# Kernel optimization log

Measured on AMD Instinct MI355X. Metric: run time of the kernel, lower is better.

The kernel has to match this reference:

```python
import jax, jax.numpy as jnp
import numpy as np

NEG_INF = -1e30


def _rotate_half(t):
    d = t.shape[-1] // 2
    t1, t2 = t[..., :d], t[..., d:]
    return jnp.concatenate([-t2, t1], axis=-1)


def _apply_rope(t, cos, sin):
    # t: [B, H, T, D]; cos/sin: [T, D] broadcast over B, H
    return t * cos[None, None, :, :] + _rotate_half(t) * sin[None, None, :, :]


def setup_inputs() -> dict:
    key = jax.random.key(0)
    ks = jax.random.split(key, 5)
    B, T, C, H = 2, 2048, 2048, 16
    D = C // H
    x = jax.random.normal(ks[0], (B, T, C), dtype=jnp.float32)
    # RoPE tables (realistic: derived from inv freqs)
    inv_freq = 1.0 / (10000.0 ** (jnp.arange(0, D, 2, dtype=jnp.float32) / D))
    freqs = jnp.arange(T, dtype=jnp.float32)[:, None] * inv_freq[None, :]
    emb = jnp.concatenate([freqs, freqs], axis=-1)  # [T, D]
    cos, sin = jnp.cos(emb), jnp.sin(emb)
    W_attn = jax.random.normal(ks[1], (C, 3 * C), dtype=jnp.float32) * (1.0 / np.sqrt(C))
    W_proj = jax.random.normal(ks[2], (C, C), dtype=jnp.float32) * (1.0 / np.sqrt(C))
    return {"x": x, "cos": cos, "sin": sin, "W_attn": W_attn, "W_proj": W_proj}


def reference(x, cos, sin, W_attn, W_proj):
    B, T, C = x.shape
    H = 16
    D = C // H
    qkv = x @ W_attn  # [B, T, 3C]
    q, k, v = jnp.split(qkv, 3, axis=-1)
    # [B, T, C] -> [B, H, T, D]
    to_heads = lambda t: t.reshape(B, T, H, D).transpose(0, 2, 1, 3)
    q, k, v = to_heads(q), to_heads(k), to_heads(v)
    q = _apply_rope(q, cos, sin)
    k = _apply_rope(k, cos, sin)
    scale = 1.0 / np.sqrt(D).astype(np.float32)
    scores = jnp.einsum("bhqd,bhkd->bhqk", q, k) * scale
    causal = jnp.tril(jnp.ones((T, T), dtype=bool))
    scores = jnp.where(causal[None, None, :, :], scores, NEG_INF)
    attn = jax.nn.softmax(scores, axis=-1)
    out = jnp.einsum("bhqk,bhkd->bhqd", attn, v)  # [B, H, T, D]
    out = out.transpose(0, 2, 1, 3).reshape(B, T, C)
    return out @ W_proj
```

## Files before the change

### kernel.cpp

```cpp
#include <hip/hip_runtime.h>
#include <stdint.h>

#define Bc   2
#define Tc   2048
#define Cc   2048
#define Hc   16
#define Dc   128
#define BT   4096
#define N3   6144
#define QSCALE 0.08838834764831845f

typedef _Float16 f16x8 __attribute__((ext_vector_type(8)));
typedef _Float16 f16x4 __attribute__((ext_vector_type(4)));
typedef float    f32x4 __attribute__((ext_vector_type(4)));

__device__ __forceinline__ void gload_lds16(const void* g, void* l) {
  __builtin_amdgcn_global_load_lds(
      (__attribute__((address_space(1))) void*)(uintptr_t)g,
      (__attribute__((address_space(3))) void*)(unsigned int)(uintptr_t)l,
      16, 0, 0);
}

__global__ __launch_bounds__(256) void cvt_f16_kernel(const float* __restrict__ in,
                                                      _Float16* __restrict__ out, int n4) {
  int i = blockIdx.x * 256 + threadIdx.x;
  if (i < n4) {
    float4 v = ((const float4*)in)[i];
    f16x4 o; o[0]=(_Float16)v.x; o[1]=(_Float16)v.y; o[2]=(_Float16)v.z; o[3]=(_Float16)v.w;
    ((f16x4*)out)[i] = o;
  }
}

__global__ __launch_bounds__(256) void transpose_cvt_kernel(const float* __restrict__ W,
                                                            _Float16* __restrict__ Wt,
                                                            int K, int N) {
  const int n0 = blockIdx.x * 64, k0 = blockIdx.y * 64;
  __shared__ float tile[64][65];
  const int tid = threadIdx.x;
  #pragma unroll
  for (int i = 0; i < 4; ++i) {
    int u = i * 256 + tid, r = u >> 4, s = u & 15;
    float4 v = *(const float4*)&W[(size_t)(k0 + r) * N + n0 + s * 4];
    tile[r][s*4+0] = v.x; tile[r][s*4+1] = v.y; tile[r][s*4+2] = v.z; tile[r][s*4+3] = v.w;
  }
  __syncthreads();
  #pragma unroll
  for (int i = 0; i < 2; ++i) {
    int u = i * 256 + tid, c = u >> 3, rg = u & 7;
    f16x8 o;
    #pragma unroll
    for (int j = 0; j < 8; ++j) o[j] = (_Float16)tile[rg * 8 + j][c];
    *(f16x8*)&Wt[(size_t)(n0 + c) * K + k0 + rg * 8] = o;
  }
}

#define GLDS_BUF 49152

template<bool OUT16>
__global__ __launch_bounds__(512, 1) void gemm256_kernel(const _Float16* __restrict__ A,
                                                         const _Float16* __restrict__ Bt,
                                                         void* __restrict__ C,
                                                         int M, int N, int K) {
  __shared__ __align__(16) char glds[3 * GLDS_BUF];
  const int tid = threadIdx.x;
  const int wid = tid >> 6, lane = tid & 63, g = lane >> 4, c16 = lane & 15;
  const int wr = wid >> 1, wc = wid & 1;

  const int nblocks = gridDim.x, chunk = nblocks >> 3;
  const int bid = blockIdx.x;
  const int sw = (bid & 7) * chunk + (bid >> 3);
  const int ntm = M >> 8;
  const int m0 = (sw % ntm) * 256, n0 = (sw / ntm) * 128;

  const int ntk = K >> 6;
  const int row8 = tid >> 3, s8 = tid & 7;
  const int scol = (s8 ^ (row8 & 7)) * 8;
  const int swz = (c16 & 7) << 4;

  auto stage_tile = [&](char* bb, int kt) {
    #pragma unroll
    for (int c = 0; c < 4; ++c)
      gload_lds16(A + (size_t)(m0 + c * 64 + row8) * K + kt * 64 + scol,
                  bb + c * 8192 + tid * 16);
    #pragma unroll
    for (int c = 0; c < 2; ++c)
      gload_lds16(Bt + (size_t)(n0 + c * 64 + row8) * K + kt * 64 + scol,
                  bb + 32768 + c * 8192 + tid * 16);
  };

  f32x4 acc[4][4] = {};

  char* p0 = glds;
  char* p1 = glds + GLDS_BUF;
  char* p2 = glds + 2 * GLDS_BUF;
  stage_tile(p0, 0);
  stage_tile(p1, 1);

  for (int t = 0; t < ntk; ++t) {
    if (t < ntk - 1) asm volatile("s_waitcnt vmcnt(6)" ::: "memory");
    else             asm volatile("s_waitcnt vmcnt(0)" ::: "memory");
    __builtin_amdgcn_s_barrier();

    f16x8 a0[4], b0[4];
    #pragma unroll
    for (int mi = 0; mi < 4; ++mi)
      a0[mi] = *(const f16x8*)(p0 + (wr * 64 + mi * 16 + c16) * 128 + ((g * 16) ^ swz));
    #pragma unroll
    for (int ni = 0; ni < 4; ++ni)
      b0[ni] = *(const f16x8*)(p0 + 32768 + (wc * 64 + ni * 16 + c16) * 128 + ((g * 16) ^ swz));
    __builtin_amdgcn_s_setprio(1);
    #pragma unroll
    for (int mi = 0; mi < 4; ++mi)
      #pragma unroll
      for (int ni = 0; ni < 4; ++ni)
        acc[mi][ni] = __builtin_amdgcn_mfma_f32_16x16x32_f16(a0[mi], b0[ni], acc[mi][ni], 0, 0, 0);
    __builtin_amdgcn_s_setprio(0);
    asm volatile("s_waitcnt lgkmcnt(0)" ::: "memory");
    __builtin_amdgcn_sched_barrier(0);
    __builtin_amdgcn_s_barrier();

    if (t + 2 < ntk) stage_tile(p2, t + 2);

    f16x8 a1[4], b1[4];
    #pragma unroll
    for (int mi = 0; mi < 4; ++mi)
      a1[mi] = *(const f16x8*)(p0 + (wr * 64 + mi * 16 + c16) * 128 + ((64 + g * 16) ^ swz));
    #pragma unroll
    for (int ni = 0; ni < 4; ++ni)
      b1[ni] = *(const f16x8*)(p0 + 32768 + (wc * 64 + ni * 16 + c16) * 128 + ((64 + g * 16) ^ swz));
    __builtin_amdgcn_s_setprio(1);
    #pragma unroll
    for (int mi = 0; mi < 4; ++mi)
      #pragma unroll
      for (int ni = 0; ni < 4; ++ni)
        acc[mi][ni] = __builtin_amdgcn_mfma_f32_16x16x32_f16(a1[mi], b1[ni], acc[mi][ni], 0, 0, 0);
    __builtin_amdgcn_s_setprio(0);
    asm volatile("s_waitcnt lgkmcnt(0)" ::: "memory");
    __builtin_amdgcn_sched_barrier(0);

    char* tp = p0; p0 = p1; p1 = p2; p2 = tp;
  }

  #pragma unroll
  for (int mi = 0; mi < 4; ++mi)
    #pragma unroll
    for (int ni = 0; ni < 4; ++ni) {
      int row = m0 + wr * 64 + mi * 16 + g * 4;
      int col = n0 + wc * 64 + ni * 16 + c16;
      #pragma unroll
      for (int r = 0; r < 4; ++r) {
        if constexpr (OUT16) ((_Float16*)C)[(size_t)(row + r) * N + col] = (_Float16)acc[mi][ni][r];
        else                 ((float*)C)[(size_t)(row + r) * N + col]    = acc[mi][ni][r];
      }
    }
}

__global__ __launch_bounds__(256) void rope_qk_kernel(const _Float16* __restrict__ qkv,
                                                      const float* __restrict__ cosT,
                                                      const float* __restrict__ sinT,
                                                      _Float16* __restrict__ Qr,
                                                      _Float16* __restrict__ Kr) {
  const int bt = blockIdx.x;
  const int b = bt >> 11, t = bt & 2047;
  const int tid = threadIdx.x;
  const _Float16* row = qkv + (size_t)bt * N3;
  const int sw = (t & 7) * 8;
  #pragma unroll
  for (int i = 0; i < 4; ++i) {
    int p = i * 256 + tid;
    int h = p >> 6, d = p & 63;
    float cs = cosT[t * Dc + d], sn = sinT[t * Dc + d];
    float ql = (float)row[h * Dc + d],        qh = (float)row[h * Dc + d + 64];
    float kl = (float)row[Cc + h * Dc + d],   kh = (float)row[Cc + h * Dc + d + 64];
    float q0 = ql * cs - qh * sn, q1 = qh * cs + ql * sn;
    float k0 = kl * cs - kh * sn, k1 = kh * cs + kl * sn;
    size_t obase = ((size_t)(b * Hc + h) * Tc + t) * Dc;
    Qr[obase + d]        = (_Float16)(q0 * QSCALE);
    Qr[obase + d + 64]   = (_Float16)(q1 * QSCALE);
    Kr[obase + (d ^ sw)]        = (_Float16)k0;
    Kr[obase + ((d + 64) ^ sw)] = (_Float16)k1;
  }
}

__global__ __launch_bounds__(256) void vtrans_kernel(const _Float16* __restrict__ qkv,
                                                     _Float16* __restrict__ Vt) {
  const int t0 = blockIdx.x * 64, d0 = blockIdx.y * 64, bh = blockIdx.z;
  const int b = bh >> 4, h = bh & 15;
  __shared__ __align__(16) _Float16 tile[64][72];
  const int tid = threadIdx.x;
  #pragma unroll
  for (int i = 0; i < 2; ++i) {
    int u = i * 256 + tid, tr = u >> 3, sg = u & 7;
    f16x8 v = *(const f16x8*)&qkv[((size_t)b * Tc + t0 + tr) * N3 + 2 * Cc + h * Dc + d0 + sg * 8];
    *(f16x8*)&tile[tr][sg * 8] = v;
  }
  __syncthreads();
  #pragma unroll
  for (int i = 0; i < 2; ++i) {
    int u = i * 256 + tid, dl = u >> 3, tg = u & 7;
    int d = d0 + dl;
    f16x8 o;
    #pragma unroll
    for (int j = 0; j < 8; ++j) o[j] = tile[tg * 8 + j][dl];
    size_t off = ((size_t)bh * Dc + d) * Tc + t0 + ((tg ^ (d & 7)) * 8);
    *(f16x8*)&Vt[off] = o;
  }
}

__global__ __launch_bounds__(256, 2) void attn_kernel(const _Float16* __restrict__ Qr,
                                                      const _Float16* __restrict__ Kr,
                                                      const _Float16* __restrict__ Vt,
                                                      _Float16* __restrict__ Oh) {
  const int bh = blockIdx.x;
  const int pr = blockIdx.y;
  const int qtA = pr, qtB = 31 - pr;
  const int tid = threadIdx.x;
  const int w = tid >> 6, lane = tid & 63, g = lane >> 4, c16 = lane & 15, l7 = lane & 7;
  const int rA = qtA * 64 + w * 16;
  const int rB = qtB * 64 + w * 16;

  __shared__ __align__(16) _Float16 Klds[2][64 * 128];
  __shared__ __align__(16) _Float16 Vlds[2][128 * 64];
  __shared__ __align__(16) _Float16 Plds[4][16][72];

  const _Float16* Qb = Qr + (size_t)bh * Tc * Dc;
  f16x8 qfA[4], qfB[4];
  #pragma unroll
  for (int kb = 0; kb < 4; ++kb) {
    qfA[kb] = *(const f16x8*)&Qb[(size_t)(rA + c16) * Dc + kb * 32 + g * 8];
    qfB[kb] = *(const f16x8*)&Qb[(size_t)(rB + c16) * Dc + kb * 32 + g * 8];
  }

  f32x4 accA[8] = {}, accB[8] = {};
  float mA[4], lA[4], mB[4], lB[4];
  #pragma unroll
  for (int r = 0; r < 4; ++r) { mA[r] = -1e30f; lA[r] = 0.f; mB[r] = -1e30f; lB[r] = 0.f; }

  const _Float16* Kt0 = Kr + (size_t)bh * Tc * Dc;

  auto stage = [&](int j, int buf) {
    const char* src = (const char*)(Kt0 + (size_t)j * 64 * Dc);
    #pragma unroll
    for (int i = 0; i < 4; ++i) {
      int ch = i * 4 + w;
      gload_lds16(src + ch * 1024 + lane * 16, (char*)(&Klds[buf][0]) + ch * 1024);
    }
    #pragma unroll
    for (int i = 0; i < 4; ++i) {
      int ch = i * 4 + w;
      int d = ch * 8 + (lane >> 3);
      const char* gs = (const char*)(Vt + ((size_t)bh * Dc + d) * Tc + j * 64) + (lane & 7) * 16;
      gload_lds16(gs, (char*)(&Vlds[buf][0]) + ch * 1024);
    }
  };

  auto process_tile = [&](f32x4* s, f32x4* acc, float* m, float* l,
                          int rT, int j, int cur, bool maskit) {
    if (maskit) {
      #pragma unroll
      for (int ni = 0; ni < 4; ++ni)
        #pragma unroll
        for (int r = 0; r < 4; ++r) {
          int q = rT + g * 4 + r;
          int kv = j * 64 + ni * 16 + c16;
          if (kv > q) s[ni][r] = -1e30f;
        }
    }
    #pragma unroll
    for (int r = 0; r < 4; ++r) {
      float mt = fmaxf(fmaxf(s[0][r], s[1][r]), fmaxf(s[2][r], s[3][r]));
      #pragma unroll
      for (int off = 1; off < 16; off <<= 1) mt = fmaxf(mt, __shfl_xor(mt, off));
      float mnew = fmaxf(m[r], mt);
      float alpha = __expf(m[r] - mnew);
      float p0 = __expf(s[0][r] - mnew), p1 = __expf(s[1][r] - mnew);
      float p2 = __expf(s[2][r] - mnew), p3 = __expf(s[3][r] - mnew);
      float ls = p0 + p1 + p2 + p3;
      #pragma unroll
      for (int off = 1; off < 16; off <<= 1) ls += __shfl_xor(ls, off);
      l[r] = l[r] * alpha + ls;
      m[r] = mnew;
      #pragma unroll
      for (int di = 0; di < 8; ++di) acc[di][r] *= alpha;
      int prow = g * 4 + r;
      Plds[w][prow][0  + c16] = (_Float16)p0;
      Plds[w][prow][16 + c16] = (_Float16)p1;
      Plds[w][prow][32 + c16] = (_Float16)p2;
      Plds[w][prow][48 + c16] = (_Float16)p3;
    }
    #pragma unroll
    for (int kvb = 0; kvb < 2; ++kvb) {
      f16x8 pf = *(const f16x8*)&Plds[w][c16][kvb * 32 + g * 8];
      __builtin_amdgcn_s_setprio(1);
      #pragma unroll
      for (int di = 0; di < 8; ++di) {
        f16x8 vf = *(const f16x8*)&Vlds[cur][(di * 16 + c16) * 64 + ((kvb * 4 + g) ^ l7) * 8];
        acc[di] = __builtin_amdgcn_mfma_f32_16x16x32_f16(pf, vf, acc[di], 0, 0, 0);
      }
      __builtin_amdgcn_s_setprio(0);
    }
  };

  const int nt = qtB + 1;
  stage(0, 0);
  __syncthreads();
  int cur = 0;
  for (int j = 0; j < nt; ++j) {
    if (j + 1 < nt) stage(j + 1, cur ^ 1);
    const bool doA = (j <= qtA);

    f32x4 sA[4] = {}, sB[4] = {};
    #pragma unroll
    for (int kb = 0; kb < 4; ++kb) {
      f16x8 bfr[4];
      #pragma unroll
      for (int ni = 0; ni < 4; ++ni)
        bfr[ni] = *(const f16x8*)&Klds[cur][(ni * 16 + c16) * 128 + ((kb * 4 + g) ^ l7) * 8];
      __builtin_amdgcn_s_setprio(1);
      #pragma unroll
      for (int ni = 0; ni < 4; ++ni) {
        sB[ni] = __builtin_amdgcn_mfma_f32_16x16x32_f16(qfB[kb], bfr[ni], sB[ni], 0, 0, 0);
        if (doA)
          sA[ni] = __builtin_amdgcn_mfma_f32_16x16x32_f16(qfA[kb], bfr[ni], sA[ni], 0, 0, 0);
      }
      __builtin_amdgcn_s_setprio(0);
    }

    process_tile(sB, accB, mB, lB, rB, j, cur, j == qtB);
    if (doA) process_tile(sA, accA, mA, lA, rA, j, cur, j == qtA);

    __syncthreads();
    cur ^= 1;
  }

  const int b = bh >> 4, h = bh & 15;
  #pragma unroll
  for (int tile = 0; tile < 2; ++tile) {
    f32x4* acc = tile ? accB : accA;
    float* l   = tile ? lB   : lA;
    int rT     = tile ? rB   : rA;
    #pragma unroll
    for (int r = 0; r < 4; ++r) {
      float inv = 1.0f / l[r];
      int trow = rT + g * 4 + r;
      _Float16* orow = Oh + ((size_t)b * Tc + trow) * Cc + h * Dc;
      #pragma unroll
      for (int di = 0; di < 8; ++di)
        orow[di * 16 + c16] = (_Float16)(acc[di][r] * inv);
    }
  }
}

extern "C" void kernel_launch(void* const* d_in, const int* in_sizes, int n_in,
                              void* d_out, int out_size, void* d_ws, size_t ws_size,
                              hipStream_t stream) {
  const float* x      = (const float*)d_in[0];
  const float* cosT   = (const float*)d_in[1];
  const float* sinT   = (const float*)d_in[2];
  const float* W_attn = (const float*)d_in[3];
  const float* W_proj = (const float*)d_in[4];
  float* out = (float*)d_out;

  const size_t OFF_XH   = 0;
  const size_t OFF_WAH  = 16777216;
  const size_t OFF_WPH  = 41943040;
  const size_t OFF_QKV  = 50331648;
  const size_t OFF_QR   = 100663296;
  const size_t OFF_KR   = 117440512;
  const size_t OFF_VT   = 134217728;
  const size_t WS_NEEDED = 150994944;
  if (ws_size < WS_NEEDED) return;

  char* ws = (char*)d_ws;
  _Float16* xh   = (_Float16*)(ws + OFF_XH);
  _Float16* Wah  = (_Float16*)(ws + OFF_WAH);
  _Float16* Wph  = (_Float16*)(ws + OFF_WPH);
  _Float16* qkvh = (_Float16*)(ws + OFF_QKV);
  _Float16* Qr   = (_Float16*)(ws + OFF_QR);
  _Float16* Kr   = (_Float16*)(ws + OFF_KR);
  _Float16* Vt   = (_Float16*)(ws + OFF_VT);
  _Float16* Oh   = qkvh;

  cvt_f16_kernel<<<dim3(8192), dim3(256), 0, stream>>>(x, xh, (Bc * Tc * Cc) / 4);
  transpose_cvt_kernel<<<dim3(N3 / 64, Cc / 64), dim3(256), 0, stream>>>(W_attn, Wah, Cc, N3);
  transpose_cvt_kernel<<<dim3(Cc / 64, Cc / 64), dim3(256), 0, stream>>>(W_proj, Wph, Cc, Cc);
  gemm256_kernel<true><<<dim3((BT / 256) * (N3 / 128)), dim3(512), 0, stream>>>(xh, Wah, qkvh, BT, N3, Cc);
  rope_qk_kernel<<<dim3(BT), dim3(256), 0, stream>>>(qkvh, cosT, sinT, Qr, Kr);
  vtrans_kernel<<<dim3(Tc / 64, Dc / 64, Bc * Hc), dim3(256), 0, stream>>>(qkvh, Vt);
  attn_kernel<<<dim3(Bc * Hc, 16), dim3(256), 0, stream>>>(Qr, Kr, Vt, Oh);
  gemm256_kernel<false><<<dim3((BT / 256) * (Cc / 128)), dim3(512), 0, stream>>>(Oh, Wph, out, BT, Cc, Cc);
}
```

Before: 421.9 us.

## Split GEMM k-step into four phases interleaving global prefetch with MFMA

Restructures the GEMM main loop so each k-tile runs in four smaller phases. Each phase loads part of the A/B fragments from LDS, issues a slice of the next-next tile's global-to-LDS loads, and then runs a subset of MFMAs. The aim is to spread memory traffic across compute and keep the matrix units busier than with one bulk prefetch in the middle. The cost is more workgroup barriers per iteration and tighter ordering constraints between the waves.

```diff
diff --git a/kernel.cpp b/kernel.cpp
--- a/kernel.cpp
+++ b/kernel.cpp
@@ -77,15 +77,13 @@
   const int scol = (s8 ^ (row8 & 7)) * 8;
   const int swz = (c16 & 7) << 4;
 
-  auto stage_tile = [&](char* bb, int kt) {
-    #pragma unroll
-    for (int c = 0; c < 4; ++c)
-      gload_lds16(A + (size_t)(m0 + c * 64 + row8) * K + kt * 64 + scol,
-                  bb + c * 8192 + tid * 16);
-    #pragma unroll
-    for (int c = 0; c < 2; ++c)
-      gload_lds16(Bt + (size_t)(n0 + c * 64 + row8) * K + kt * 64 + scol,
-                  bb + 32768 + c * 8192 + tid * 16);
+  auto stageA = [&](char* bb, int kt, int c) {
+    gload_lds16(A + (size_t)(m0 + c * 64 + row8) * K + kt * 64 + scol,
+                bb + c * 8192 + tid * 16);
+  };
+  auto stageB = [&](char* bb, int kt, int c) {
+    gload_lds16(Bt + (size_t)(n0 + c * 64 + row8) * K + kt * 64 + scol,
+                bb + 32768 + c * 8192 + tid * 16);
   };
 
   f32x4 acc[4][4] = {};
@@ -93,50 +91,93 @@
   char* p0 = glds;
   char* p1 = glds + GLDS_BUF;
   char* p2 = glds + 2 * GLDS_BUF;
-  stage_tile(p0, 0);
-  stage_tile(p1, 1);
+  #pragma unroll
+  for (int c = 0; c < 4; ++c) stageA(p0, 0, c);
+  #pragma unroll
+  for (int c = 0; c < 2; ++c) stageB(p0, 0, c);
+  #pragma unroll
+  for (int c = 0; c < 4; ++c) stageA(p1, 1, c);
+  #pragma unroll
+  for (int c = 0; c < 2; ++c) stageB(p1, 1, c);
+
+  const int arow = wr * 64 + c16;
+  const int brow = wc * 64 + c16;
 
   for (int t = 0; t < ntk; ++t) {
     if (t < ntk - 1) asm volatile("s_waitcnt vmcnt(6)" ::: "memory");
     else             asm volatile("s_waitcnt vmcnt(0)" ::: "memory");
     __builtin_amdgcn_s_barrier();
-
-    f16x8 a0[4], b0[4];
-    #pragma unroll
-    for (int mi = 0; mi < 4; ++mi)
-      a0[mi] = *(const f16x8*)(p0 + (wr * 64 + mi * 16 + c16) * 128 + ((g * 16) ^ swz));
-    #pragma unroll
-    for (int ni = 0; ni < 4; ++ni)
-      b0[ni] = *(const f16x8*)(p0 + 32768 + (wc * 64 + ni * 16 + c16) * 128 + ((g * 16) ^ swz));
+    const bool st = (t + 2 < ntk);
+
+    f16x8 a0[4], b0[4], a1[4], b1[4];
+
+    #pragma unroll
+    for (int mi = 0; mi < 4; ++mi)
+      a0[mi] = *(const f16x8*)(p0 + (arow + mi * 16) * 128 + ((g * 16) ^ swz));
+    #pragma unroll
+    for (int ni = 0; ni < 2; ++ni)
+      b0[ni] = *(const f16x8*)(p0 + 32768 + (brow + ni * 16) * 128 + ((g * 16) ^ swz));
+    if (st) { stageA(p2, t + 2, 0); stageA(p2, t + 2, 1); }
+    __builtin_amdgcn_s_barrier();
+    asm volatile("s_waitcnt lgkmcnt(0)" ::: "memory");
+    __builtin_amdgcn_sched_barrier(0);
     __builtin_amdgcn_s_setprio(1);
     #pragma unroll
     for (int mi = 0; mi < 4; ++mi)
       #pragma unroll
-      for (int ni = 0; ni < 4; ++ni)
+      for (int ni = 0; ni < 2; ++ni)
         acc[mi][ni] = __builtin_amdgcn_mfma_f32_16x16x32_f16(a0[mi], b0[ni], acc[mi][ni], 0, 0, 0);
     __builtin_amdgcn_s_setprio(0);
+    __builtin_amdgcn_s_barrier();
+
+    #pragma unroll
+    for (int ni = 2; ni < 4; ++ni)
+      b0[ni] = *(const f16x8*)(p0 + 32768 + (brow + ni * 16) * 128 + ((g * 16) ^ swz));
+    if (st) { stageA(p2, t + 2, 2); stageA(p2, t + 2, 3); }
+    __builtin_amdgcn_s_barrier();
     asm volatile("s_waitcnt lgkmcnt(0)" ::: "memory");
     __builtin_amdgcn_sched_barrier(0);
-    __builtin_amdgcn_s_barrier();
-
-    if (t + 2 < ntk) stage_tile(p2, t + 2);
-
-    f16x8 a1[4], b1[4];
-    #pragma unroll
-    for (int mi = 0; mi < 4; ++mi)
-      a1[mi] = *(const f16x8*)(p0 + (wr * 64 + mi * 16 + c16) * 128 + ((64 + g * 16) ^ swz));
-    #pragma unroll
-    for (int ni = 0; ni < 4; ++ni)
-      b1[ni] = *(const f16x8*)(p0 + 32768 + (wc * 64 + ni * 16 + c16) * 128 + ((64 + g * 16) ^ swz));
     __builtin_amdgcn_s_setprio(1);
     #pragma unroll
     for (int mi = 0; mi < 4; ++mi)
       #pragma unroll
-      for (int ni = 0; ni < 4; ++ni)
+      for (int ni = 2; ni < 4; ++ni)
+        acc[mi][ni] = __builtin_amdgcn_mfma_f32_16x16x32_f16(a0[mi], b0[ni], acc[mi][ni], 0, 0, 0);
+    __builtin_amdgcn_s_setprio(0);
+    __builtin_amdgcn_s_barrier();
+
+    #pragma unroll
+    for (int mi = 0; mi < 4; ++mi)
+      a1[mi] = *(const f16x8*)(p0 + (arow + mi * 16) * 128 + ((64 + g * 16) ^ swz));
+    #pragma unroll
+    for (int ni = 0; ni < 2; ++ni)
+      b1[ni] = *(const f16x8*)(p0 + 32768 + (brow + ni * 16) * 128 + ((64 + g * 16) ^ swz));
+    if (st) { stageB(p2, t + 2, 0); stageB(p2, t + 2, 1); }
+    __builtin_amdgcn_s_barrier();
+    asm volatile("s_waitcnt lgkmcnt(0)" ::: "memory");
+    __builtin_amdgcn_sched_barrier(0);
+    __builtin_amdgcn_s_setprio(1);
+    #pragma unroll
+    for (int mi = 0; mi < 4; ++mi)
+      #pragma unroll
+      for (int ni = 0; ni < 2; ++ni)
         acc[mi][ni] = __builtin_amdgcn_mfma_f32_16x16x32_f16(a1[mi], b1[ni], acc[mi][ni], 0, 0, 0);
     __builtin_amdgcn_s_setprio(0);
+    __builtin_amdgcn_s_barrier();
+
+    #pragma unroll
+    for (int ni = 2; ni < 4; ++ni)
+      b1[ni] = *(const f16x8*)(p0 + 32768 + (brow + ni * 16) * 128 + ((64 + g * 16) ^ swz));
+    __builtin_amdgcn_s_barrier();
     asm volatile("s_waitcnt lgkmcnt(0)" ::: "memory");
     __builtin_amdgcn_sched_barrier(0);
+    __builtin_amdgcn_s_setprio(1);
+    #pragma unroll
+    for (int mi = 0; mi < 4; ++mi)
+      #pragma unroll
+      for (int ni = 2; ni < 4; ++ni)
+        acc[mi][ni] = __builtin_amdgcn_mfma_f32_16x16x32_f16(a1[mi], b1[ni], acc[mi][ni], 0, 0, 0);
+    __builtin_amdgcn_s_setprio(0);
 
     char* tp = p0; p0 = p1; p1 = p2; p2 = tp;
   }
```

Measured after the change: 412.9 us. -2.1%, faster.
